# Performance work log

Measured on AMD Instinct MI355X. Metric: run time of the kernel, lower is better.

Reference implementation:

```python
import jax, jax.numpy as jnp
import numpy as np

B, S, D = 2, 4096, 512
H, DQK, DV, W = 8, 64, 64, 32
ORDER = 6  # 2^(2*6)=4096 cells: 64x64 Hilbert grid covers max_seq_len=4096


def hilbert_d2xy(d, order):
    """Vectorized standard Hilbert curve d->(x,y) mapping on a 2^order grid."""
    x = jnp.zeros_like(d)
    y = jnp.zeros_like(d)
    t = d
    s = 1
    for _ in range(order):
        rx = (t // 2) & 1
        ry = (t ^ rx) & 1
        swap = ry == 0
        flip = swap & (rx == 1)
        xf = jnp.where(flip, s - 1 - x, x)
        yf = jnp.where(flip, s - 1 - y, y)
        x, y = jnp.where(swap, yf, xf), jnp.where(swap, xf, yf)
        x = x + s * rx
        y = y + s * ry
        t = t // 4
        s = s * 2
    return jnp.stack([x, y], axis=-1)


def neighbor_idx(seq_len, window):
    d = jnp.arange(seq_len, dtype=jnp.int32)
    coords = hilbert_d2xy(d, ORDER).astype(jnp.float32)  # (S, 2)
    diff = coords[:, None, :] - coords[None, :, :]
    dist = jnp.sqrt((diff ** 2).sum(-1))  # (S, S)
    _, idx = jax.lax.top_k(-dist, window)  # k smallest distances
    return idx.astype(jnp.int32)


def setup_inputs() -> dict:
    key = jax.random.key(0)
    k1, k2, k3, k4, k5 = jax.random.split(key, 5)
    sc = float(1.0 / np.sqrt(D))
    return {
        "x": jax.random.normal(k1, (B, S, D), jnp.float32),
        "W_q": jax.random.normal(k2, (H * DQK, D), jnp.float32) * sc,
        "W_k": jax.random.normal(k3, (H * DQK, D), jnp.float32) * sc,
        "W_v": jax.random.normal(k4, (H * DV, D), jnp.float32) * sc,
        "W_o": jax.random.normal(k5, (D, H * DV), jnp.float32) * sc,
        "neighbor_indices": neighbor_idx(S, W),
    }


def reference(x, W_q, W_k, W_v, W_o, neighbor_indices):
    b, s, _ = x.shape
    q = (x @ W_q.T).reshape(b, s, H, DQK).transpose(0, 2, 1, 3)  # (b,h,s,d)
    k = (x @ W_k.T).reshape(b, s, H, DQK).transpose(0, 2, 1, 3)
    v = (x @ W_v.T).reshape(b, s, H, DV).transpose(0, 2, 1, 3)
    kn = k[:, :, neighbor_indices, :]  # gather -> (b,h,s,w,d)
    vn = v[:, :, neighbor_indices, :]
    scale = float(1.0 / np.sqrt(DQK))
    scores = jnp.einsum('bhsd,bhswd->bhsw', q, kn) * scale
    attn = jax.nn.softmax(scores, axis=-1)
    out = jnp.einsum('bhsw,bhswd->bhsd', attn, vn)
    out = out.transpose(0, 2, 1, 3).reshape(b, s, H * DV)
    return out @ W_o.T
```

## Files before the change

### kernel.cpp

```cpp
#include <hip/hip_runtime.h>
#include <hip/hip_bf16.h>
#include <stdint.h>
#include <stddef.h>

constexpr int Bc = 2;
constexpr int Sc = 4096;
constexpr int Dc = 512;
constexpr int Hc = 8;
constexpr int Wc = 32;

using bf16_t = __bf16;
using f16_t  = _Float16;
typedef __attribute__((ext_vector_type(8))) __bf16 bf16x8;
typedef __attribute__((ext_vector_type(4))) __bf16 bf16x4;
typedef __attribute__((ext_vector_type(2))) __bf16 bf16x2;
typedef __attribute__((ext_vector_type(8))) _Float16 f16x8;
typedef __attribute__((ext_vector_type(2))) _Float16 f16x2;
typedef __attribute__((ext_vector_type(4))) float f32x4;

__device__ __forceinline__ void async_copy16(const void* g, void* l) {
    __builtin_amdgcn_global_load_lds(
        (const __attribute__((address_space(1))) void*)g,
        (__attribute__((address_space(3))) void*)l,
        16, 0, 0);
}

__global__ void convert_all(const float* __restrict__ x,
                            const float* __restrict__ wq, const float* __restrict__ wk,
                            const float* __restrict__ wv, const float* __restrict__ wo,
                            bf16_t* __restrict__ xc, bf16_t* __restrict__ dq,
                            bf16_t* __restrict__ dk, bf16_t* __restrict__ dv,
                            bf16_t* __restrict__ dwo) {
    const int blk = blockIdx.x;
    const float* s; bf16_t* d; int base;
    if (blk < 4096) { s = x; d = xc; base = blk * 1024; }
    else {
        const int r = blk - 4096, which = r >> 8;
        s = (which == 0) ? wq : (which == 1) ? wk : (which == 2) ? wv : wo;
        d = (which == 0) ? dq : (which == 1) ? dk : (which == 2) ? dv : dwo;
        base = (r & 255) * 1024;
    }
    const int i = base + threadIdx.x * 4;
    const float4 v = *(const float4*)(s + i);
    bf16x4 o; o[0] = (bf16_t)v.x; o[1] = (bf16_t)v.y;
    o[2] = (bf16_t)v.z; o[3] = (bf16_t)v.w;
    *(bf16x4*)(d + i) = o;
}

template<int BM, int BN, int TM, int TN, int OMODE>
__global__ __launch_bounds__(256) void gemm_bt(
    const bf16_t* __restrict__ A, int lda,
    const bf16_t* __restrict__ B0, const bf16_t* __restrict__ B1,
    const bf16_t* __restrict__ B2, int ldb, int nPerB,
    void* __restrict__ C, int ldc, int K)
{
    constexpr int BK = 32;
    __shared__ __align__(1024) bf16_t Alds[BM * BK];
    __shared__ __align__(1024) bf16_t Blds[BN * BK];

    const int tid  = threadIdx.x;
    const int lane = tid & 63;
    const int wv   = tid >> 6;
    const int wm   = wv >> 1;
    const int wn   = wv & 1;
    const int r    = lane & 15;
    const int q4   = lane >> 4;

    const int blkM = blockIdx.x * BM;
    const int colC = blockIdx.y * BN;

    const bf16_t* Bp = B0;
    int nB = colC;
    if (nPerB > 0) {
        int wsel = colC / nPerB;
        nB = colC - wsel * nPerB;
        Bp = (wsel == 0) ? B0 : (wsel == 1) ? B1 : B2;
    }

    f32x4 acc[TM][TN];
    const f32x4 fzero = {0.f, 0.f, 0.f, 0.f};
    #pragma unroll
    for (int i = 0; i < TM; ++i)
        #pragma unroll
        for (int j = 0; j < TN; ++j) acc[i][j] = fzero;

    constexpr int A_LOADS = (BM * BK * 2) / (256 * 16);
    constexpr int B_LOADS = (BN * BK * 2) / (256 * 16);

    for (int kk = 0; kk < K; kk += BK) {
        __syncthreads();
        #pragma unroll
        for (int i = 0; i < A_LOADS; ++i) {
            int off  = i * 4096 + tid * 16;
            int row  = off >> 6;
            int colb = off & 63;
            const char* g = (const char*)A + ((size_t)(blkM + row) * lda + kk) * 2 + colb;
            async_copy16(g, (char*)Alds + off);
        }
        #pragma unroll
        for (int i = 0; i < B_LOADS; ++i) {
            int off  = i * 4096 + tid * 16;
            int row  = off >> 6;
            int colb = off & 63;
            const char* g = (const char*)Bp + ((size_t)(nB + row) * ldb + kk) * 2 + colb;
            async_copy16(g, (char*)Blds + off);
        }
        __syncthreads();

        bf16x8 af[TM], bfr[TN];
        #pragma unroll
        for (int mt = 0; mt < TM; ++mt)
            af[mt] = *(const bf16x8*)&Alds[(wm * TM * 16 + mt * 16 + r) * BK + q4 * 8];
        #pragma unroll
        for (int nt = 0; nt < TN; ++nt)
            bfr[nt] = *(const bf16x8*)&Blds[(wn * TN * 16 + nt * 16 + r) * BK + q4 * 8];

        #pragma unroll
        for (int mt = 0; mt < TM; ++mt)
            #pragma unroll
            for (int nt = 0; nt < TN; ++nt)
                acc[mt][nt] = __builtin_amdgcn_mfma_f32_16x16x32_bf16(
                    af[mt], bfr[nt], acc[mt][nt], 0, 0, 0);
    }

    #pragma unroll
    for (int mt = 0; mt < TM; ++mt) {
        #pragma unroll
        for (int nt = 0; nt < TN; ++nt) {
            int rr0 = blkM + wm * TM * 16 + mt * 16 + q4 * 4;
            int cc  = colC + wn * TN * 16 + nt * 16 + r;
            #pragma unroll
            for (int i = 0; i < 4; ++i) {
                size_t o = (size_t)(rr0 + i) * ldc + cc;
                if constexpr (OMODE == 1)      ((float*)C)[o]  = acc[mt][nt][i];
                else if constexpr (OMODE == 2) ((f16_t*)C)[o]  = (f16_t)acc[mt][nt][i];
                else                           ((bf16_t*)C)[o] = (bf16_t)acc[mt][nt][i];
            }
        }
    }
}

__global__ __launch_bounds__(256) void attn_fast(
    const f16_t* __restrict__ QKV,
    const int*   __restrict__ nidx,
    bf16_t*      __restrict__ attn_out)
{
    __shared__ __align__(16) float wa_lds[4][64];
    const int lane = threadIdx.x & 63;
    const int wv   = threadIdx.x >> 6;

    const int bi  = blockIdx.x;
    const int blk = (bi & 7) * 2048 + (bi >> 3);
    const int wg  = blk * 4 + wv;
    const int s = wg & (Sc - 1);
    const int h = (wg >> 12) & (Hc - 1);
    const int b = wg >> 15;
    const size_t row = (size_t)b * Sc + s;

    const int w    = lane >> 1;
    const int half = lane & 1;
    const int t    = nidx[s * Wc + w];

    const char* qkvB = (const char*)QKV;
    const char* Qptr = qkvB + row * 3072 + h * 128 + half * 64;
    const char* Kptr = qkvB + ((size_t)b * Sc + t) * 3072 + 1024 + h * 128 + half * 64;

    f16x8 q8[4], k8[4];
    #pragma unroll
    for (int i = 0; i < 4; ++i) {
        q8[i] = *(const f16x8*)(Qptr + 16 * i);
        k8[i] = *(const f16x8*)(Kptr + 16 * i);
    }
    float p = 0.f;
    #pragma unroll
    for (int i = 0; i < 4; ++i) {
        #pragma unroll
        for (int j = 0; j < 4; ++j) {
            f16x2 qa; qa[0] = q8[i][2 * j]; qa[1] = q8[i][2 * j + 1];
            f16x2 kb; kb[0] = k8[i][2 * j]; kb[1] = k8[i][2 * j + 1];
            p = __builtin_amdgcn_fdot2(qa, kb, p, false);
        }
    }
    p += __shfl_xor(p, 1);
    p *= 0.125f;

    float mx = p;
    #pragma unroll
    for (int m = 2; m <= 32; m <<= 1) mx = fmaxf(mx, __shfl_xor(mx, m));
    const float e = __expf(p - mx);
    float sum = e;
    #pragma unroll
    for (int m = 2; m <= 32; m <<= 1) sum += __shfl_xor(sum, m);
    const float a = e / sum;

    if (half == 0) {
        wa_lds[wv][2 * w]     = __int_as_float(t * 3072);
        wa_lds[wv][2 * w + 1] = a;
    }
    __syncthreads();

    const int d2 = lane & 31;
    const int nh = lane >> 5;
    const float* chunkp = &wa_lds[wv][nh * 32];
    const char* Vb = qkvB + (size_t)b * Sc * 3072 + 2048 + h * 128;
    const int dk = d2 * 4;

    float acc0 = 0.f, acc1 = 0.f;
    #pragma unroll
    for (int j = 0; j < 8; ++j) {
        const float4 c = *(const float4*)(chunkp + 4 * j);
        {
            const unsigned v = *(const unsigned*)(Vb + __float_as_int(c.x) + dk);
            const f16x2 v2 = __builtin_bit_cast(f16x2, v);
            acc0 = fmaf(c.y, (float)v2[0], acc0);
            acc1 = fmaf(c.y, (float)v2[1], acc1);
        }
        {
            const unsigned v = *(const unsigned*)(Vb + __float_as_int(c.z) + dk);
            const f16x2 v2 = __builtin_bit_cast(f16x2, v);
            acc0 = fmaf(c.w, (float)v2[0], acc0);
            acc1 = fmaf(c.w, (float)v2[1], acc1);
        }
    }
    acc0 += __shfl_xor(acc0, 32);
    acc1 += __shfl_xor(acc1, 32);
    if (nh == 0) {
        bf16x2 pr; pr[0] = (bf16_t)acc0; pr[1] = (bf16_t)acc1;
        *(bf16x2*)((char*)attn_out + row * 1024 + h * 128 + dk) = pr;
    }
}

extern "C" void kernel_launch(void* const* d_in, const int* in_sizes, int n_in,
                              void* d_out, int out_size, void* d_ws, size_t ws_size,
                              hipStream_t stream) {
    (void)in_sizes; (void)n_in; (void)out_size; (void)ws_size;
    const int* nidx = (const int*)d_in[5];
    const int M = Bc * Sc;
    float* out = (float*)d_out;

    char* w = (char*)d_ws;
    bf16_t* xc   = (bf16_t*)(w + 256);
    bf16_t* Wqc  = xc  + 4194304;
    bf16_t* Wkc  = Wqc + 262144;
    bf16_t* Wvc  = Wkc + 262144;
    bf16_t* Woc  = Wvc + 262144;
    f16_t*  qkv  = (f16_t*)(Woc + 262144);
    bf16_t* attnS = xc;

    convert_all<<<5120, 256, 0, stream>>>(
        (const float*)d_in[0], (const float*)d_in[1], (const float*)d_in[2],
        (const float*)d_in[3], (const float*)d_in[4],
        xc, Wqc, Wkc, Wvc, Woc);

    gemm_bt<128, 128, 4, 4, 2><<<dim3(M / 128, 1536 / 128), 256, 0, stream>>>(
        xc, Dc, Wqc, Wkc, Wvc, Dc, 512, qkv, 1536, Dc);

    attn_fast<<<(Bc * Hc * Sc) / 4, 256, 0, stream>>>(qkv, nidx, attnS);

    gemm_bt<128, 64, 4, 2, 1><<<dim3(M / 128, 512 / 64), 256, 0, stream>>>(
        attnS, 512, Woc, Woc, Woc, 512, 0, out, Dc, Dc);
}
```

Baseline: 150.3 us.

## Double GEMM K-step per sync and give each attention wave two queries

The GEMM now loads two 32-wide K slabs into separate LDS buffers per iteration, which halves the number of barrier pairs per tile while doubling LDS use. The attention kernel now has each wave handle two query positions, one lane per neighbor, computing the full 64-dim dot product per lane. It drops the max-subtraction in the softmax and the cross-half shuffle reductions, and removes the reduction in the V accumulation. Skipping max subtraction risks overflow for large scores, and each lane now carries heavier per-lane loads of 128 bytes each for Q and K.

```diff
diff --git a/kernel.cpp b/kernel.cpp
--- a/kernel.cpp
+++ b/kernel.cpp
@@ -14,7 +14,6 @@
 typedef __attribute__((ext_vector_type(8))) __bf16 bf16x8;
 typedef __attribute__((ext_vector_type(4))) __bf16 bf16x4;
 typedef __attribute__((ext_vector_type(2))) __bf16 bf16x2;
-typedef __attribute__((ext_vector_type(8))) _Float16 f16x8;
 typedef __attribute__((ext_vector_type(2))) _Float16 f16x2;
 typedef __attribute__((ext_vector_type(4))) float f32x4;
 
@@ -48,15 +47,14 @@
 }
 
 template<int BM, int BN, int TM, int TN, int OMODE>
-__global__ __launch_bounds__(256) void gemm_bt(
+__global__ __launch_bounds__(256) void gemm_bt2(
     const bf16_t* __restrict__ A, int lda,
     const bf16_t* __restrict__ B0, const bf16_t* __restrict__ B1,
     const bf16_t* __restrict__ B2, int ldb, int nPerB,
     void* __restrict__ C, int ldc, int K)
 {
-    constexpr int BK = 32;
-    __shared__ __align__(1024) bf16_t Alds[BM * BK];
-    __shared__ __align__(1024) bf16_t Blds[BN * BK];
+    __shared__ __align__(1024) bf16_t Alds[2][BM * 32];
+    __shared__ __align__(1024) bf16_t Blds[2][BN * 32];
 
     const int tid  = threadIdx.x;
     const int lane = tid & 63;
@@ -84,43 +82,51 @@
         #pragma unroll
         for (int j = 0; j < TN; ++j) acc[i][j] = fzero;
 
-    constexpr int A_LOADS = (BM * BK * 2) / (256 * 16);
-    constexpr int B_LOADS = (BN * BK * 2) / (256 * 16);
-
-    for (int kk = 0; kk < K; kk += BK) {
+    constexpr int A_LOADS = (BM * 32 * 2) / (256 * 16);
+    constexpr int B_LOADS = (BN * 32 * 2) / (256 * 16);
+
+    for (int kk = 0; kk < K; kk += 64) {
         __syncthreads();
         #pragma unroll
-        for (int i = 0; i < A_LOADS; ++i) {
-            int off  = i * 4096 + tid * 16;
-            int row  = off >> 6;
-            int colb = off & 63;
-            const char* g = (const char*)A + ((size_t)(blkM + row) * lda + kk) * 2 + colb;
-            async_copy16(g, (char*)Alds + off);
-        }
-        #pragma unroll
-        for (int i = 0; i < B_LOADS; ++i) {
-            int off  = i * 4096 + tid * 16;
-            int row  = off >> 6;
-            int colb = off & 63;
-            const char* g = (const char*)Bp + ((size_t)(nB + row) * ldb + kk) * 2 + colb;
-            async_copy16(g, (char*)Blds + off);
+        for (int p = 0; p < 2; ++p) {
+            #pragma unroll
+            for (int i = 0; i < A_LOADS; ++i) {
+                int off  = i * 4096 + tid * 16;
+                int row  = off >> 6;
+                int colb = off & 63;
+                const char* g = (const char*)A +
+                    ((size_t)(blkM + row) * lda + kk + p * 32) * 2 + colb;
+                async_copy16(g, (char*)Alds[p] + off);
+            }
+            #pragma unroll
+            for (int i = 0; i < B_LOADS; ++i) {
+                int off  = i * 4096 + tid * 16;
+                int row  = off >> 6;
+                int colb = off & 63;
+                const char* g = (const char*)Bp +
+                    ((size_t)(nB + row) * ldb + kk + p * 32) * 2 + colb;
+                async_copy16(g, (char*)Blds[p] + off);
+            }
         }
         __syncthreads();
 
-        bf16x8 af[TM], bfr[TN];
-        #pragma unroll
-        for (int mt = 0; mt < TM; ++mt)
-            af[mt] = *(const bf16x8*)&Alds[(wm * TM * 16 + mt * 16 + r) * BK + q4 * 8];
-        #pragma unroll
-        for (int nt = 0; nt < TN; ++nt)
-            bfr[nt] = *(const bf16x8*)&Blds[(wn * TN * 16 + nt * 16 + r) * BK + q4 * 8];
-
-        #pragma unroll
-        for (int mt = 0; mt < TM; ++mt)
+        #pragma unroll
+        for (int ks = 0; ks < 2; ++ks) {
+            bf16x8 af[TM], bfr[TN];
+            #pragma unroll
+            for (int mt = 0; mt < TM; ++mt)
+                af[mt] = *(const bf16x8*)&Alds[ks][(wm * TM * 16 + mt * 16 + r) * 32 + q4 * 8];
             #pragma unroll
             for (int nt = 0; nt < TN; ++nt)
-                acc[mt][nt] = __builtin_amdgcn_mfma_f32_16x16x32_bf16(
-                    af[mt], bfr[nt], acc[mt][nt], 0, 0, 0);
+                bfr[nt] = *(const bf16x8*)&Blds[ks][(wn * TN * 16 + nt * 16 + r) * 32 + q4 * 8];
+
+            #pragma unroll
+            for (int mt = 0; mt < TM; ++mt)
+                #pragma unroll
+                for (int nt = 0; nt < TN; ++nt)
+                    acc[mt][nt] = __builtin_amdgcn_mfma_f32_16x16x32_bf16(
+                        af[mt], bfr[nt], acc[mt][nt], 0, 0, 0);
+        }
     }
 
     #pragma unroll
@@ -140,94 +146,84 @@
     }
 }
 
-__global__ __launch_bounds__(256) void attn_fast(
+__global__ __launch_bounds__(256) void attn_pair(
     const f16_t* __restrict__ QKV,
     const int*   __restrict__ nidx,
     bf16_t*      __restrict__ attn_out)
 {
-    __shared__ __align__(16) float wa_lds[4][64];
+    __shared__ __align__(16) float wa_lds[4][128];
     const int lane = threadIdx.x & 63;
     const int wv   = threadIdx.x >> 6;
 
     const int bi  = blockIdx.x;
-    const int blk = (bi & 7) * 2048 + (bi >> 3);
+    const int blk = (bi & 7) * 1024 + (bi >> 3);
     const int wg  = blk * 4 + wv;
-    const int s = wg & (Sc - 1);
-    const int h = (wg >> 12) & (Hc - 1);
-    const int b = wg >> 15;
-    const size_t row = (size_t)b * Sc + s;
-
-    const int w    = lane >> 1;
-    const int half = lane & 1;
-    const int t    = nidx[s * Wc + w];
+    const int sp = wg & 2047;
+    const int h  = (wg >> 11) & 7;
+    const int b  = wg >> 14;
+
+    const int sw = lane >> 5;
+    const int w  = lane & 31;
+    const int s  = 2 * sp + sw;
+    const int t  = nidx[s * Wc + w];
 
     const char* qkvB = (const char*)QKV;
-    const char* Qptr = qkvB + row * 3072 + h * 128 + half * 64;
-    const char* Kptr = qkvB + ((size_t)b * Sc + t) * 3072 + 1024 + h * 128 + half * 64;
-
-    f16x8 q8[4], k8[4];
-    #pragma unroll
-    for (int i = 0; i < 4; ++i) {
-        q8[i] = *(const f16x8*)(Qptr + 16 * i);
-        k8[i] = *(const f16x8*)(Kptr + 16 * i);
-    }
-    float p = 0.f;
-    #pragma unroll
-    for (int i = 0; i < 4; ++i) {
-        #pragma unroll
-        for (int j = 0; j < 4; ++j) {
-            f16x2 qa; qa[0] = q8[i][2 * j]; qa[1] = q8[i][2 * j + 1];
-            f16x2 kb; kb[0] = k8[i][2 * j]; kb[1] = k8[i][2 * j + 1];
-            p = __builtin_amdgcn_fdot2(qa, kb, p, false);
-        }
-    }
-    p += __shfl_xor(p, 1);
-    p *= 0.125f;
-
-    float mx = p;
-    #pragma unroll
-    for (int m = 2; m <= 32; m <<= 1) mx = fmaxf(mx, __shfl_xor(mx, m));
-    const float e = __expf(p - mx);
+    const char* Qp = qkvB + ((size_t)b * Sc + s) * 3072 + h * 128;
+    const char* Kp = qkvB + ((size_t)b * Sc + t) * 3072 + 1024 + h * 128;
+
+    uint4 qv[8], kv[8];
+    #pragma unroll
+    for (int i = 0; i < 8; ++i) {
+        qv[i] = *(const uint4*)(Qp + 16 * i);
+        kv[i] = *(const uint4*)(Kp + 16 * i);
+    }
+    float p0 = 0.f, p1 = 0.f;
+    #pragma unroll
+    for (int i = 0; i < 8; ++i) {
+        p0 = __builtin_amdgcn_fdot2(__builtin_bit_cast(f16x2, qv[i].x),
+                                    __builtin_bit_cast(f16x2, kv[i].x), p0, false);
+        p1 = __builtin_amdgcn_fdot2(__builtin_bit_cast(f16x2, qv[i].y),
+                                    __builtin_bit_cast(f16x2, kv[i].y), p1, false);
+        p0 = __builtin_amdgcn_fdot2(__builtin_bit_cast(f16x2, qv[i].z),
+                                    __builtin_bit_cast(f16x2, kv[i].z), p0, false);
+        p1 = __builtin_amdgcn_fdot2(__builtin_bit_cast(f16x2, qv[i].w),
+                                    __builtin_bit_cast(f16x2, kv[i].w), p1, false);
+    }
+    const float e = __expf((p0 + p1) * 0.125f);
     float sum = e;
     #pragma unroll
-    for (int m = 2; m <= 32; m <<= 1) sum += __shfl_xor(sum, m);
+    for (int m = 1; m <= 16; m <<= 1) sum += __shfl_xor(sum, m);
     const float a = e / sum;
 
-    if (half == 0) {
-        wa_lds[wv][2 * w]     = __int_as_float(t * 3072);
-        wa_lds[wv][2 * w + 1] = a;
+    {
+        float2 wr; wr.x = __int_as_float(t * 3072); wr.y = a;
+        *(float2*)&wa_lds[wv][2 * lane] = wr;
     }
     __syncthreads();
 
     const int d2 = lane & 31;
-    const int nh = lane >> 5;
-    const float* chunkp = &wa_lds[wv][nh * 32];
-    const char* Vb = qkvB + (size_t)b * Sc * 3072 + 2048 + h * 128;
-    const int dk = d2 * 4;
+    const float* ch = &wa_lds[wv][sw * 64];
+    const char* Vp = qkvB + (size_t)b * Sc * 3072 + 2048 + h * 128 + d2 * 4;
 
     float acc0 = 0.f, acc1 = 0.f;
     #pragma unroll
-    for (int j = 0; j < 8; ++j) {
-        const float4 c = *(const float4*)(chunkp + 4 * j);
+    for (int j = 0; j < 16; ++j) {
+        const float4 c = *(const float4*)(ch + 4 * j);
         {
-            const unsigned v = *(const unsigned*)(Vb + __float_as_int(c.x) + dk);
+            const unsigned v = *(const unsigned*)(Vp + __float_as_int(c.x));
             const f16x2 v2 = __builtin_bit_cast(f16x2, v);
             acc0 = fmaf(c.y, (float)v2[0], acc0);
             acc1 = fmaf(c.y, (float)v2[1], acc1);
         }
         {
-            const unsigned v = *(const unsigned*)(Vb + __float_as_int(c.z) + dk);
+            const unsigned v = *(const unsigned*)(Vp + __float_as_int(c.z));
             const f16x2 v2 = __builtin_bit_cast(f16x2, v);
             acc0 = fmaf(c.w, (float)v2[0], acc0);
             acc1 = fmaf(c.w, (float)v2[1], acc1);
         }
     }
-    acc0 += __shfl_xor(acc0, 32);
-    acc1 += __shfl_xor(acc1, 32);
-    if (nh == 0) {
-        bf16x2 pr; pr[0] = (bf16_t)acc0; pr[1] = (bf16_t)acc1;
-        *(bf16x2*)((char*)attn_out + row * 1024 + h * 128 + dk) = pr;
-    }
+    bf16x2 pr; pr[0] = (bf16_t)acc0; pr[1] = (bf16_t)acc1;
+    *(bf16x2*)((char*)attn_out + ((size_t)b * Sc + s) * 1024 + h * 128 + d2 * 4) = pr;
 }
 
 extern "C" void kernel_launch(void* const* d_in, const int* in_sizes, int n_in,
@@ -252,11 +248,11 @@
         (const float*)d_in[3], (const float*)d_in[4],
         xc, Wqc, Wkc, Wvc, Woc);
 
-    gemm_bt<128, 128, 4, 4, 2><<<dim3(M / 128, 1536 / 128), 256, 0, stream>>>(
+    gemm_bt2<128, 128, 4, 4, 2><<<dim3(M / 128, 1536 / 128), 256, 0, stream>>>(
         xc, Dc, Wqc, Wkc, Wvc, Dc, 512, qkv, 1536, Dc);
 
-    attn_fast<<<(Bc * Hc * Sc) / 4, 256, 0, stream>>>(qkv, nidx, attnS);
-
-    gemm_bt<128, 64, 4, 2, 1><<<dim3(M / 128, 512 / 64), 256, 0, stream>>>(
+    attn_pair<<<(Bc * Hc * Sc) / 8, 256, 0, stream>>>(qkv, nidx, attnS);
+
+    gemm_bt2<128, 64, 4, 2, 1><<<dim3(M / 128, 512 / 64), 256, 0, stream>>>(
         attnS, 512, Woc, Woc, Woc, 512, 0, out, Dc, Dc);
 }
```

After: 159.2 us. +5.9%, slower.
